# Performance work log

Measured on AMD Instinct MI355X. Metric: run time of the kernel, lower is better.

## Reference

```python
import jax, jax.numpy as jnp
import numpy as np


def setup_inputs() -> dict:
    key = jax.random.key(0)
    ks = jax.random.split(key, 5)
    B, S, D = 2, 2048, 1024
    std = 0.02
    return {
        "x": jax.random.normal(ks[0], (B, S, D), dtype=jnp.float32),
        "Wq": jax.random.normal(ks[1], (D, D), dtype=jnp.float32) * std,
        "Wk": jax.random.normal(ks[2], (D, D), dtype=jnp.float32) * std,
        "Wv": jax.random.normal(ks[3], (D, D), dtype=jnp.float32) * std,
        "Wo": jax.random.normal(ks[4], (D, D), dtype=jnp.float32) * std,
        "num_heads": 16,
        "window_size": 512,
    }


def reference(x, Wq, Wk, Wv, Wo, num_heads, window_size):
    B, S, D = x.shape
    H = num_heads
    d = D // H
    scale = d ** (-0.5)

    # QKV projections (torch Linear: y = x @ W.T), split heads -> b h s d
    def proj(W):
        return (x @ W.T).reshape(B, S, H, d).transpose(0, 2, 1, 3)

    q, k, v = proj(Wq), proj(Wk), proj(Wv)

    # [B, H, S, S] scores (faithful to the dense SDPA fallback)
    scores = jnp.einsum("bhsd,bhtd->bhst", q, k) * scale

    # sliding-window causal mask: col <= row and row - col < window_size
    pos = jnp.arange(S)
    row, col = pos[:, None], pos[None, :]
    mask = (col <= row) & (row - col < window_size)  # [S, S]
    scores = jnp.where(mask[None, None], scores, -jnp.inf)

    attn = jax.nn.softmax(scores, axis=-1)
    out = jnp.einsum("bhst,bhtd->bhsd", attn, v)  # b h s d
    out = out.transpose(0, 2, 1, 3).reshape(B, S, D)  # merge heads
    return out @ Wo.T
```

## Files before the change

kernel.cpp:

```cpp
#include <hip/hip_runtime.h>
#include <cstdint>

typedef uint16_t u16;
typedef __attribute__((ext_vector_type(8))) short short8;
typedef __attribute__((ext_vector_type(4))) float f32x4;

__device__ __forceinline__ u16 f2bf(float f) {
  uint32_t u = __float_as_uint(f);
  u += 0x7fff + ((u >> 16) & 1);
  return (u16)(u >> 16);
}
__device__ __forceinline__ uint32_t pk2bf(float a, float b) {
  uint32_t ua = __float_as_uint(a) + 0x8000u;
  uint32_t ub = __float_as_uint(b) + 0x8000u;
  return (ua >> 16) | (ub & 0xFFFF0000u);
}

#define GLL16(gp, lp) __builtin_amdgcn_global_load_lds( \
    (__attribute__((address_space(1))) void*)(gp), \
    (__attribute__((address_space(3))) void*)(lp), 16, 0, 0)

#define SBAR()       __builtin_amdgcn_s_barrier()
#define WAIT_LGKM0() asm volatile("s_waitcnt lgkmcnt(0)" ::: "memory")
#define WAIT_VM(N)   asm volatile("s_waitcnt vmcnt(" #N ")" ::: "memory")
#define MEMBAR()     asm volatile("" ::: "memory")

template<int N> __device__ __forceinline__ void wait_vm() {
  static_assert(N == 0 || N == 4 || N == 6 || N == 8 || N == 10 || N == 12, "add literal case");
  if constexpr (N == 0)  { WAIT_VM(0); }
  else if constexpr (N == 4)  { WAIT_VM(4); }
  else if constexpr (N == 6)  { WAIT_VM(6); }
  else if constexpr (N == 8)  { WAIT_VM(8); }
  else if constexpr (N == 10) { WAIT_VM(10); }
  else if constexpr (N == 12) { WAIT_VM(12); }
}

__global__ void cvt_all(const float* __restrict__ x,  const float* __restrict__ wq,
                        const float* __restrict__ wk, const float* __restrict__ wv,
                        const float* __restrict__ wo,
                        u16* __restrict__ xb, u16* __restrict__ wcat, u16* __restrict__ wob) {
  int i = blockIdx.x * 256 + threadIdx.x;
  const float4* src; ushort4* dst; int off; float sc = 1.0f;
  if (i < 1048576)      { src = (const float4*)x;  dst = (ushort4*)xb;              off = i; }
  else if (i < 1310720) { src = (const float4*)wq; dst = (ushort4*)wcat;            off = i - 1048576;
                          sc = 0.18033688011112042f; }
  else if (i < 1572864) { src = (const float4*)wk; dst = (ushort4*)wcat + 262144;   off = i - 1310720; }
  else if (i < 1835008) { src = (const float4*)wv; dst = (ushort4*)wcat + 524288;   off = i - 1572864; }
  else                  { src = (const float4*)wo; dst = (ushort4*)wob;             off = i - 1835008; }
  float4 v = src[off];
  ushort4 o;
  o.x = f2bf(v.x * sc); o.y = f2bf(v.y * sc); o.z = f2bf(v.z * sc); o.w = f2bf(v.w * sc);
  dst[off] = o;
}

template<int BM, int BN, int OUT_BF16>
__global__ __launch_bounds__(256, 2) void gemm_t(const u16* __restrict__ A,
                                                 const u16* __restrict__ B,
                                                 void* __restrict__ Cout,
                                                 int N, int K, int ntN) {
  constexpr int MF = BM / 32;
  constexpr int NF = BN / 32;
  constexpr int G  = (BM + BN) / 32;
  __shared__ u16 smA[2][BM * 64];
  __shared__ u16 smB[2][BN * 64];
  const int tid  = threadIdx.x;
  const int lane = tid & 63, w = tid >> 6;
  const int wr = w >> 1, wc = w & 1;
  const int g = lane >> 4, lr = lane & 15;

  const int cpx = gridDim.x >> 3;
  const int id  = blockIdx.x;
  const int sw  = (id & 7) * cpx + (id >> 3);
  const int row0 = (sw / ntN) * BM, col0 = (sw % ntN) * BN;
  const int T = K >> 6;

  f32x4 acc[MF][NF];
  #pragma unroll
  for (int i = 0; i < MF; ++i)
    #pragma unroll
    for (int j = 0; j < NF; ++j) acc[i][j] = (f32x4){0.f, 0.f, 0.f, 0.f};

  auto STAGE = [&](int kt, int bufi) {
    #pragma unroll
    for (int j = 0; j < BM / 32; ++j) {
      int r  = j * 32 + w * 8 + (lane >> 3);
      int sb = ((lane & 7) << 4) ^ ((r & 7) << 4);
      GLL16(A + (size_t)(row0 + r) * K + kt * 64 + (sb >> 1),
            &smA[bufi][(size_t)(j * 32 + w * 8) * 64]);
    }
    #pragma unroll
    for (int j = 0; j < BN / 32; ++j) {
      int r  = j * 32 + w * 8 + (lane >> 3);
      int sb = ((lane & 7) << 4) ^ ((r & 7) << 4);
      GLL16(B + (size_t)(col0 + r) * K + kt * 64 + (sb >> 1),
            &smB[bufi][(size_t)(j * 32 + w * 8) * 64]);
    }
  };

  STAGE(0, 0); STAGE(1, 1);
  wait_vm<G>(); SBAR(); MEMBAR();

  for (int t = 0; t < T; ++t) {
    const int cur = t & 1;
    short8 a[MF][2], b[NF][2];
    #pragma unroll
    for (int mm = 0; mm < MF; ++mm)
      #pragma unroll
      for (int kh = 0; kh < 2; ++kh) {
        int row = wr * (BM / 2) + mm * 16 + lr;
        int col = (kh * 64 + g * 16) ^ ((row & 7) << 4);
        a[mm][kh] = *(const short8*)((const char*)&smA[cur][0] + row * 128 + col);
      }
    #pragma unroll
    for (int nn = 0; nn < NF; ++nn)
      #pragma unroll
      for (int kh = 0; kh < 2; ++kh) {
        int row = wc * (BN / 2) + nn * 16 + lr;
        int col = (kh * 64 + g * 16) ^ ((row & 7) << 4);
        b[nn][kh] = *(const short8*)((const char*)&smB[cur][0] + row * 128 + col);
      }
    WAIT_LGKM0(); MEMBAR(); SBAR(); MEMBAR();

    if (t + 2 < T) STAGE(t + 2, cur);

    __builtin_amdgcn_s_setprio(1);
    #pragma unroll
    for (int kh = 0; kh < 2; ++kh)
      #pragma unroll
      for (int mm = 0; mm < MF; ++mm)
        #pragma unroll
        for (int nn = 0; nn < NF; ++nn)
          acc[mm][nn] = __builtin_amdgcn_mfma_f32_16x16x32_bf16(
              a[mm][kh], b[nn][kh], acc[mm][nn], 0, 0, 0);
    __builtin_amdgcn_s_setprio(0);

    if (t + 1 < T) {
      if (t + 2 < T) { wait_vm<G>(); } else { wait_vm<0>(); }
      SBAR(); MEMBAR();
    }
  }

  #pragma unroll
  for (int i = 0; i < MF; ++i)
    #pragma unroll
    for (int j = 0; j < NF; ++j)
      #pragma unroll
      for (int ri = 0; ri < 4; ++ri) {
        int rr = row0 + wr * (BM / 2) + i * 16 + g * 4 + ri;
        int cc = col0 + wc * (BN / 2) + j * 16 + lr;
        if (OUT_BF16) ((u16*)Cout)[(size_t)rr * N + cc] = f2bf(acc[i][j][ri]);
        else          ((float*)Cout)[(size_t)rr * N + cc] = acc[i][j][ri];
      }
}

__global__ __launch_bounds__(512, 4) void attn_swa(const u16* __restrict__ QKV, u16* __restrict__ O) {
  const int S = 2048;
  const int qb = blockIdx.x * 128;
  const int b = blockIdx.y >> 4, h = blockIdx.y & 15;
  const int tid = threadIdx.x;
  const int lane = tid & 63, w = tid >> 6;
  const int g = lane >> 4, lr = lane & 15;

  __shared__ u16 Klds[2][64 * 64];
  __shared__ u16 Vt[2][64][72];
  __shared__ u16 Plds[8][16][72];

  const u16* Qb = QKV + (size_t)b * S * 3072 + h * 64;
  const u16* Kb = QKV + (size_t)b * S * 3072 + 1024 + h * 64;
  const u16* Vb = QKV + (size_t)b * S * 3072 + 2048 + h * 64;

  const int qw = qb + w * 16;
  short8 qf[2];
  #pragma unroll
  for (int kh = 0; kh < 2; ++kh)
    qf[kh] = *(const short8*)(Qb + (size_t)(qw + lr) * 3072 + kh * 32 + g * 8);

  float ls = 0.f;
  f32x4 accO[4];
  #pragma unroll
  for (int i = 0; i < 4; ++i) accO[i] = (f32x4){0.f, 0.f, 0.f, 0.f};

  int ks = qb - 511; if (ks < 0) ks = 0; ks &= ~63;
  const int ke = qb + 127;
  const int nt = ((ke - ks) >> 6) + 1;

  short8 vreg;

  auto STAGE_K = [&](int kb, int buf) {
    int r  = w * 8 + (lane >> 3);
    int sb = ((lane & 7) << 4) ^ ((r & 7) << 4);
    const u16* gp = Kb + (size_t)(kb + r) * 3072 + (sb >> 1);
    u16* lp = Klds[buf] + w * 512;
    GLL16(gp, lp);
  };
  auto LOAD_V = [&](int kb) {
    vreg = *(const short8*)(Vb + (size_t)(kb + lane) * 3072 + w * 8);
  };
  auto WRITE_V = [&](int buf) {
    #pragma unroll
    for (int j = 0; j < 8; ++j) Vt[buf][w * 8 + j][lane] = (u16)vreg[j];
  };

  LOAD_V(ks); MEMBAR();
  STAGE_K(ks, 0); MEMBAR();
  WAIT_VM(0); MEMBAR();
  SBAR(); MEMBAR();
  WRITE_V(0);

  int cur = 0, kb = ks;
  for (int t = 0; t < nt; ++t, kb += 64) {
    const int nxt = cur ^ 1;
    const bool more = (t + 1 < nt);
    if (more) { LOAD_V(kb + 64); MEMBAR(); STAGE_K(kb + 64, nxt); MEMBAR(); }

    const bool active = (kb <= qw + 15) && (kb + 63 >= qw - 511);
    if (active) {
      float p[4][4];
      #pragma unroll
      for (int st = 0; st < 4; ++st) {
        f32x4 c4 = (f32x4){0.f, 0.f, 0.f, 0.f};
        int r = st * 16 + lr;
        int swz = (r & 7) << 4;
        const char* krow = (const char*)(Klds[cur]) + r * 128;
        short8 kf0 = *(const short8*)(krow + ((g * 16) ^ swz));
        short8 kf1 = *(const short8*)(krow + ((64 + g * 16) ^ swz));
        __builtin_amdgcn_s_setprio(1);
        c4 = __builtin_amdgcn_mfma_f32_16x16x32_bf16(kf0, qf[0], c4, 0, 0, 0);
        c4 = __builtin_amdgcn_mfma_f32_16x16x32_bf16(kf1, qf[1], c4, 0, 0, 0);
        __builtin_amdgcn_s_setprio(0);
        #pragma unroll
        for (int ri = 0; ri < 4; ++ri) p[st][ri] = c4[ri];
      }

      const bool clean = (kb + 63 <= qw) && (qw + 15 - kb < 512);
      if (clean) {
        #pragma unroll
        for (int st = 0; st < 4; ++st)
          #pragma unroll
          for (int ri = 0; ri < 4; ++ri)
            p[st][ri] = __builtin_amdgcn_exp2f(p[st][ri]);
      } else {
        const int base = qw + lr - kb;
        #pragma unroll
        for (int st = 0; st < 4; ++st)
          #pragma unroll
          for (int ri = 0; ri < 4; ++ri) {
            float e = __builtin_amdgcn_exp2f(p[st][ri]);
            p[st][ri] = ((uint32_t)(base - (st * 16 + g * 4 + ri)) < 512u) ? e : 0.f;
          }
      }
      {
        float s = 0.f;
        #pragma unroll
        for (int st = 0; st < 4; ++st)
          #pragma unroll
          for (int ri = 0; ri < 4; ++ri) s += p[st][ri];
        s += __shfl_xor(s, 16);
        s += __shfl_xor(s, 32);
        ls += s;
      }
      #pragma unroll
      for (int st = 0; st < 4; ++st) {
        uint2 u2;
        u2.x = pk2bf(p[st][0], p[st][1]);
        u2.y = pk2bf(p[st][2], p[st][3]);
        *(uint2*)(&Plds[w][lr][st * 16 + g * 4]) = u2;
      }
    }

    if (more) { WAIT_VM(0); MEMBAR(); }
    WAIT_LGKM0(); MEMBAR();
    SBAR(); MEMBAR();
    if (more) WRITE_V(nxt);

    if (active) {
      short8 pf0 = *(const short8*)(&Plds[w][lr][g * 8]);
      short8 pf1 = *(const short8*)(&Plds[w][lr][32 + g * 8]);
      __builtin_amdgcn_s_setprio(1);
      #pragma unroll
      for (int dt = 0; dt < 4; ++dt) {
        short8 vf0 = *(const short8*)(&Vt[cur][dt * 16 + lr][g * 8]);
        short8 vf1 = *(const short8*)(&Vt[cur][dt * 16 + lr][32 + g * 8]);
        accO[dt] = __builtin_amdgcn_mfma_f32_16x16x32_bf16(pf0, vf0, accO[dt], 0, 0, 0);
        accO[dt] = __builtin_amdgcn_mfma_f32_16x16x32_bf16(pf1, vf1, accO[dt], 0, 0, 0);
      }
      __builtin_amdgcn_s_setprio(0);
    }
    cur = nxt;
  }

  float lsq[4];
  #pragma unroll
  for (int ri = 0; ri < 4; ++ri) lsq[ri] = __shfl(ls, g * 4 + ri);
  #pragma unroll
  for (int dt = 0; dt < 4; ++dt)
    #pragma unroll
    for (int ri = 0; ri < 4; ++ri) {
      int qi = qw + g * 4 + ri;
      O[(size_t)(b * S + qi) * 1024 + h * 64 + dt * 16 + lr] = f2bf(accO[dt][ri] / lsq[ri]);
    }
}

extern "C" void kernel_launch(void* const* d_in, const int* in_sizes, int n_in,
                              void* d_out, int out_size, void* d_ws, size_t ws_size,
                              hipStream_t stream) {
  const float* x  = (const float*)d_in[0];
  const float* Wq = (const float*)d_in[1];
  const float* Wk = (const float*)d_in[2];
  const float* Wv = (const float*)d_in[3];
  const float* Wo = (const float*)d_in[4];

  char* ws = (char*)d_ws;
  u16* xb   = (u16*)(ws);
  u16* Wcat = (u16*)(ws + (8  << 20));
  u16* Wob  = (u16*)(ws + (14 << 20));
  u16* QKV  = (u16*)(ws + (16 << 20));
  u16* Oatt = (u16*)(ws + (40 << 20));

  cvt_all<<<8192, 256, 0, stream>>>(x, Wq, Wk, Wv, Wo, xb, Wcat, Wob);
  gemm_t<128, 192, 1><<<512, 256, 0, stream>>>(xb, Wcat, QKV, 3072, 1024, 16);
  attn_swa<<<dim3(16, 32), 512, 0, stream>>>(QKV, Oatt);
  gemm_t<64, 128, 0><<<512, 256, 0, stream>>>(Oatt, Wob, d_out, 1024, 1024, 8);
}
```

Before: 82.57 us.

## Deepen attention K/V prefetch to two tiles ahead with triple-buffered K

```diff
diff --git a/kernel.cpp b/kernel.cpp
--- a/kernel.cpp
+++ b/kernel.cpp
@@ -26,8 +26,9 @@
 #define MEMBAR()     asm volatile("" ::: "memory")
 
 template<int N> __device__ __forceinline__ void wait_vm() {
-  static_assert(N == 0 || N == 4 || N == 6 || N == 8 || N == 10 || N == 12, "add literal case");
+  static_assert(N == 0 || N == 2 || N == 4 || N == 6 || N == 8 || N == 10 || N == 12, "add literal case");
   if constexpr (N == 0)  { WAIT_VM(0); }
+  else if constexpr (N == 2)  { WAIT_VM(2); }
   else if constexpr (N == 4)  { WAIT_VM(4); }
   else if constexpr (N == 6)  { WAIT_VM(6); }
   else if constexpr (N == 8)  { WAIT_VM(8); }
@@ -161,7 +162,7 @@
   const int lane = tid & 63, w = tid >> 6;
   const int g = lane >> 4, lr = lane & 15;
 
-  __shared__ u16 Klds[2][64 * 64];
+  __shared__ u16 Klds[3][64 * 64];
   __shared__ u16 Vt[2][64][72];
   __shared__ u16 Plds[8][16][72];
 
@@ -183,8 +184,6 @@
   int ks = qb - 511; if (ks < 0) ks = 0; ks &= ~63;
   const int ke = qb + 127;
   const int nt = ((ke - ks) >> 6) + 1;
-
-  short8 vreg;
 
   auto STAGE_K = [&](int kb, int buf) {
     int r  = w * 8 + (lane >> 3);
@@ -193,25 +192,34 @@
     u16* lp = Klds[buf] + w * 512;
     GLL16(gp, lp);
   };
-  auto LOAD_V = [&](int kb) {
-    vreg = *(const short8*)(Vb + (size_t)(kb + lane) * 3072 + w * 8);
+  auto LOAD_V = [&](int kb) -> short8 {
+    return *(const short8*)(Vb + (size_t)(kb + lane) * 3072 + w * 8);
   };
-  auto WRITE_V = [&](int buf) {
-    #pragma unroll
-    for (int j = 0; j < 8; ++j) Vt[buf][w * 8 + j][lane] = (u16)vreg[j];
+  auto WRITE_V = [&](int buf, short8 v) {
+    #pragma unroll
+    for (int j = 0; j < 8; ++j) Vt[buf][w * 8 + j][lane] = (u16)v[j];
   };
 
-  LOAD_V(ks); MEMBAR();
+  short8 vrW, vrL;
+
+  vrW = LOAD_V(ks); MEMBAR();
   STAGE_K(ks, 0); MEMBAR();
-  WAIT_VM(0); MEMBAR();
+  if (nt > 1) { vrL = LOAD_V(ks + 64); MEMBAR(); STAGE_K(ks + 64, 1); MEMBAR(); }
+  if (nt > 1) { wait_vm<2>(); } else { wait_vm<0>(); }
+  MEMBAR();
   SBAR(); MEMBAR();
-  WRITE_V(0);
-
-  int cur = 0, kb = ks;
+  WRITE_V(0, vrW);
+  vrW = vrL;
+
+  int kc = 0, kb = ks;
   for (int t = 0; t < nt; ++t, kb += 64) {
-    const int nxt = cur ^ 1;
     const bool more = (t + 1 < nt);
-    if (more) { LOAD_V(kb + 64); MEMBAR(); STAGE_K(kb + 64, nxt); MEMBAR(); }
+    const bool pre  = (t + 2 < nt);
+    if (pre) {
+      vrL = LOAD_V(kb + 128); MEMBAR();
+      int kst = kc + 2; if (kst >= 3) kst -= 3;
+      STAGE_K(kb + 128, kst); MEMBAR();
+    }
 
     const bool active = (kb <= qw + 15) && (kb + 63 >= qw - 511);
     if (active) {
@@ -221,7 +229,7 @@
         f32x4 c4 = (f32x4){0.f, 0.f, 0.f, 0.f};
         int r = st * 16 + lr;
         int swz = (r & 7) << 4;
-        const char* krow = (const char*)(Klds[cur]) + r * 128;
+        const char* krow = (const char*)(Klds[kc]) + r * 128;
         short8 kf0 = *(const short8*)(krow + ((g * 16) ^ swz));
         short8 kf1 = *(const short8*)(krow + ((64 + g * 16) ^ swz));
         __builtin_amdgcn_s_setprio(1);
@@ -268,10 +276,16 @@
       }
     }
 
-    if (more) { WAIT_VM(0); MEMBAR(); }
+    if (more) {
+      if (pre) { wait_vm<2>(); } else { wait_vm<0>(); }
+      MEMBAR();
+    }
     WAIT_LGKM0(); MEMBAR();
     SBAR(); MEMBAR();
-    if (more) WRITE_V(nxt);
+    if (more) {
+      WRITE_V((t + 1) & 1, vrW);
+      vrW = vrL;
+    }
 
     if (active) {
       short8 pf0 = *(const short8*)(&Plds[w][lr][g * 8]);
@@ -279,14 +293,15 @@
       __builtin_amdgcn_s_setprio(1);
       #pragma unroll
       for (int dt = 0; dt < 4; ++dt) {
-        short8 vf0 = *(const short8*)(&Vt[cur][dt * 16 + lr][g * 8]);
-        short8 vf1 = *(const short8*)(&Vt[cur][dt * 16 + lr][32 + g * 8]);
+        short8 vf0 = *(const short8*)(&Vt[t & 1][dt * 16 + lr][g * 8]);
+        short8 vf1 = *(const short8*)(&Vt[t & 1][dt * 16 + lr][32 + g * 8]);
         accO[dt] = __builtin_amdgcn_mfma_f32_16x16x32_bf16(pf0, vf0, accO[dt], 0, 0, 0);
         accO[dt] = __builtin_amdgcn_mfma_f32_16x16x32_bf16(pf1, vf1, accO[dt], 0, 0, 0);
       }
       __builtin_amdgcn_s_setprio(0);
     }
-    cur = nxt;
+
+    ++kc; if (kc == 3) kc = 0;
   }
 
   float lsq[4];
```

Result: no change. 83.72 us (+1.4%).
